# Kernel optimization log

Hardware: AMD Instinct MI355X
Metric: run time of the kernel (lower is better)

The kernel has to match this reference:

```python
import jax, jax.numpy as jnp
import numpy as np


def setup_inputs() -> dict:
    key = jax.random.key(0)
    k1, k2, k3, k4 = jax.random.split(key, 4)
    N, D, H = 16384, 128, 256
    features = jax.random.normal(k1, (N, D), dtype=jnp.float32)
    adj_matrix = jax.random.randint(k2, (N, N), 0, 2, dtype=jnp.int32)
    # Linear(2D -> H) and Linear(D -> H), torch convention W: [out, in]
    Wd = jax.random.normal(k3, (H, 2 * D), dtype=jnp.float32) * (1.0 / np.sqrt(2 * D))
    bd = jnp.zeros((H,), dtype=jnp.float32)
    Wo = jax.random.normal(k4, (H, D), dtype=jnp.float32) * (1.0 / np.sqrt(D))
    bo = jnp.zeros((H,), dtype=jnp.float32)
    return {"features": features, "adj_matrix": adj_matrix,
            "Wd": Wd, "bd": bd, "Wo": Wo, "bo": bo}


def reference(features, adj_matrix, Wd, bd, Wo, bo):
    # Faithful math, but without materializing the O(N^2*2D) pairwise tensor:
    #   sum_j adj[i,j] * concat(f[i], f[j]) = concat(deg[i]*f[i], (adj @ f)[i])
    adj = adj_matrix.astype(features.dtype)
    deg = jnp.sum(adj, axis=-1, keepdims=True)              # [N,1]
    neigh_mask = jnp.max(adj, axis=-1, keepdims=True)       # [N,1]
    neigh_num = deg + (1.0 - neigh_mask)                    # avoid div by 0
    head_sum = features * deg                                # [N,D]
    tail_sum = adj @ features                                # [N,D]
    neigh_ave = jnp.concatenate([head_sum, tail_sum], axis=-1) / neigh_num  # [N,2D]
    neigh_feat = neigh_ave @ Wd.T + bd                       # [N,H]
    updated = (features @ Wo.T + bo) - neigh_feat            # [N,H]
    updated = jnp.tanh(updated)
    # dropout is identity in eval mode; withAgg=False returns the pair
    return (updated, updated)
```

## Files before the change

### kernel.cpp

```cpp
#include <hip/hip_runtime.h>
#include <hip/hip_bf16.h>

#define NROW 16384
#define DIM 128
#define HOUT 256
#define SPLIT 4

typedef float f32x4 __attribute__((ext_vector_type(4)));
typedef __bf16 bf16x8 __attribute__((ext_vector_type(8)));
typedef int v4i __attribute__((ext_vector_type(4)));
typedef unsigned int u32;
typedef unsigned int u32x4 __attribute__((ext_vector_type(4)));

__global__ void k_transpose(const float* __restrict__ f, short* __restrict__ fT,
                            float* __restrict__ deg) {
    __shared__ short tr[128][72];
    const int t = threadIdx.x;
    const int j0 = blockIdx.x * 64;
    if (blockIdx.x < 64) deg[blockIdx.x * 256 + t] = 0.f;
    for (int it = 0; it < 8; ++it) {
        int slot = t + 256 * it;
        int j = slot >> 5;
        int dq = slot & 31;
        f32x4 v = *reinterpret_cast<const f32x4*>(f + (size_t)(j0 + j) * DIM + dq * 4);
#pragma unroll
        for (int c = 0; c < 4; ++c) {
            __hip_bfloat16 h = __float2bfloat16(v[c]);
            tr[dq * 4 + c][j] = *reinterpret_cast<short*>(&h);
        }
    }
    __syncthreads();
    for (int it = 0; it < 4; ++it) {
        int slot = t + 256 * it;
        int d = slot >> 3;
        int c8 = slot & 7;
        int4 v = *reinterpret_cast<const int4*>(&tr[d][c8 * 8]);
        *reinterpret_cast<int4*>(fT + (size_t)d * NROW + j0 + c8 * 8) = v;
    }
}

__device__ inline bf16x8 cvt8(v4i a, v4i b, int& ds) {
    union { u32x4 u; bf16x8 f; } U;
    U.u[0] = (a[0] ? 0x3F80u : 0u) | (a[1] ? 0x3F800000u : 0u);
    U.u[1] = (a[2] ? 0x3F80u : 0u) | (a[3] ? 0x3F800000u : 0u);
    U.u[2] = (b[0] ? 0x3F80u : 0u) | (b[1] ? 0x3F800000u : 0u);
    U.u[3] = (b[2] ? 0x3F80u : 0u) | (b[3] ? 0x3F800000u : 0u);
    ds += a[0] + a[1] + a[2] + a[3] + b[0] + b[1] + b[2] + b[3];
    return U.f;
}

#define GLOAD16(g, l)                                                         \
    __builtin_amdgcn_global_load_lds(                                         \
        (const __attribute__((address_space(1))) unsigned int*)(g),           \
        (__attribute__((address_space(3))) unsigned int*)(l), 16, 0, 0)

__global__ __launch_bounds__(256, 2) void k_gemm(const int* __restrict__ adj,
                                                 const short* __restrict__ fT,
                                                 float* __restrict__ part,
                                                 float* __restrict__ deg) {
    __shared__ int   As[2][128][32];
    __shared__ short Fs[2][128][32];
    const int t = threadIdx.x;
    const int rb = blockIdx.x >> 2;
    const int s  = blockIdx.x & 3;
    const int i0 = rb * 128;
    const int kb0 = s * (NROW / SPLIT);
    const int lane = t & 63;
    const int w = t >> 6;
    const int lr = lane & 15;
    const int lk8 = lane >> 4;

    f32x4 acc[2][8] = {};
    int dsum0 = 0, dsum1 = 0;

#define STAGE(cur, kb)                                                            \
    do {                                                                          \
        _Pragma("unroll")                                                         \
        for (int r = 0; r < 4; ++r) {                                             \
            int uslot = r * 256 + w * 64;                                         \
            int slot = uslot + lane;                                              \
            const int* g = adj + (size_t)(i0 + (slot >> 3)) * NROW + (kb) + (slot & 7) * 4; \
            GLOAD16(g, (char*)&As[cur][0][0] + (size_t)uslot * 16);               \
        }                                                                         \
        _Pragma("unroll")                                                         \
        for (int r = 0; r < 2; ++r) {                                             \
            int uslot = r * 256 + w * 64;                                         \
            int slot = uslot + lane;                                              \
            const short* g = fT + (size_t)(slot >> 2) * NROW + (kb) + (slot & 3) * 8; \
            GLOAD16(g, (char*)&Fs[cur][0][0] + (size_t)uslot * 16);               \
        }                                                                         \
    } while (0)

    STAGE(0, kb0);
    __syncthreads();

    int cur = 0;
#pragma unroll 1
    for (int step = 0; step < 128; ++step) {
        if (step + 1 < 128) STAGE(cur ^ 1, kb0 + (step + 1) * 32);
        bf16x8 bfr[8];
#pragma unroll
        for (int ci = 0; ci < 8; ++ci)
            bfr[ci] = *reinterpret_cast<const bf16x8*>(&Fs[cur][ci * 16 + lr][lk8 * 8]);
        v4i a0 = *reinterpret_cast<const v4i*>(&As[cur][w * 32 + lr][lk8 * 8]);
        v4i a1 = *reinterpret_cast<const v4i*>(&As[cur][w * 32 + lr][lk8 * 8 + 4]);
        v4i a2 = *reinterpret_cast<const v4i*>(&As[cur][w * 32 + 16 + lr][lk8 * 8]);
        v4i a3 = *reinterpret_cast<const v4i*>(&As[cur][w * 32 + 16 + lr][lk8 * 8 + 4]);
        bf16x8 af0 = cvt8(a0, a1, dsum0);
        bf16x8 af1 = cvt8(a2, a3, dsum1);
#pragma unroll
        for (int ci = 0; ci < 8; ++ci) {
            acc[0][ci] = __builtin_amdgcn_mfma_f32_16x16x32_bf16(af0, bfr[ci], acc[0][ci], 0, 0, 0);
            acc[1][ci] = __builtin_amdgcn_mfma_f32_16x16x32_bf16(af1, bfr[ci], acc[1][ci], 0, 0, 0);
        }
        __syncthreads();
        cur ^= 1;
    }

#pragma unroll
    for (int ti = 0; ti < 2; ++ti)
#pragma unroll
        for (int ci = 0; ci < 8; ++ci)
#pragma unroll
            for (int r = 0; r < 4; ++r) {
                int i = i0 + w * 32 + ti * 16 + (lane >> 4) * 4 + r;
                int d = ci * 16 + lr;
                part[((size_t)s * NROW + i) * DIM + d] = acc[ti][ci][r];
            }
    {
        float v0 = (float)dsum0;
        v0 += __shfl_xor(v0, 16);
        v0 += __shfl_xor(v0, 32);
        float v1 = (float)dsum1;
        v1 += __shfl_xor(v1, 16);
        v1 += __shfl_xor(v1, 32);
        if (lane < 16) {
            atomicAdd(deg + i0 + w * 32 + lr, v0);
            atomicAdd(deg + i0 + w * 32 + 16 + lr, v1);
        }
    }
#undef STAGE
}

__global__ __launch_bounds__(256, 2) void k_epilogue(const float* __restrict__ feat,
                                                     const float* __restrict__ part,
                                                     const float* __restrict__ deg,
                                                     const float* __restrict__ Wd,
                                                     const float* __restrict__ bd,
                                                     const float* __restrict__ Wo,
                                                     const float* __restrict__ bo,
                                                     float* __restrict__ out) {
    __shared__ float fs[32][132];
    __shared__ float tn[32][132];
    __shared__ float mrow[32], inv[32];
    const int t = threadIdx.x;
    const int i0 = blockIdx.x * 32;
    if (t < 32) {
        float d = deg[i0 + t];
        mrow[t] = d > 0.f ? 1.f : 0.f;
        inv[t]  = d > 0.f ? 1.f / d : 1.f;
    }
    __syncthreads();
    for (int it = 0; it < 4; ++it) {
        int slot = t + 256 * it;
        int r = slot >> 5, dq = slot & 31;
        size_t gi = (size_t)(i0 + r) * DIM + dq * 4;
        f32x4 fv = *reinterpret_cast<const f32x4*>(feat + gi);
        *reinterpret_cast<f32x4*>(&fs[r][dq * 4]) = fv;
        f32x4 p = *reinterpret_cast<const f32x4*>(part + gi);
#pragma unroll
        for (int sp = 1; sp < SPLIT; ++sp)
            p += *reinterpret_cast<const f32x4*>(part + (size_t)sp * NROW * DIM + gi);
        f32x4 tv = p * inv[r];
        *reinterpret_cast<f32x4*>(&tn[r][dq * 4]) = tv;
    }
    __syncthreads();
    const int rt = t & 7;
    const int ht = t >> 3;
    float accM[4][8] = {};
    float accB[4][8] = {};
    for (int d = 0; d < DIM; d += 4) {
        f32x4 fr[4], tr[4];
#pragma unroll
        for (int rr = 0; rr < 4; ++rr) {
            fr[rr] = *reinterpret_cast<const f32x4*>(&fs[rt * 4 + rr][d]);
            tr[rr] = *reinterpret_cast<const f32x4*>(&tn[rt * 4 + rr][d]);
        }
#pragma unroll
        for (int hh = 0; hh < 8; ++hh) {
            int h = ht * 8 + hh;
            f32x4 wo = *reinterpret_cast<const f32x4*>(Wo + (size_t)h * DIM + d);
            f32x4 w1 = *reinterpret_cast<const f32x4*>(Wd + (size_t)h * 2 * DIM + d);
            f32x4 w2 = *reinterpret_cast<const f32x4*>(Wd + (size_t)h * 2 * DIM + DIM + d);
#pragma unroll
            for (int rr = 0; rr < 4; ++rr)
#pragma unroll
                for (int c = 0; c < 4; ++c) {
                    accM[rr][hh] += fr[rr][c] * wo[c] - tr[rr][c] * w2[c];
                    accB[rr][hh] += fr[rr][c] * w1[c];
                }
        }
    }
    f32x4 bo0 = *reinterpret_cast<const f32x4*>(bo + ht * 8);
    f32x4 bo1 = *reinterpret_cast<const f32x4*>(bo + ht * 8 + 4);
    f32x4 bd0 = *reinterpret_cast<const f32x4*>(bd + ht * 8);
    f32x4 bd1 = *reinterpret_cast<const f32x4*>(bd + ht * 8 + 4);
#pragma unroll
    for (int rr = 0; rr < 4; ++rr) {
        int i = i0 + rt * 4 + rr;
        float m = mrow[rt * 4 + rr];
        f32x4 v0, v1;
#pragma unroll
        for (int c = 0; c < 4; ++c) {
            v0[c] = tanhf(accM[rr][c]     - m * accB[rr][c]     + bo0[c] - bd0[c]);
            v1[c] = tanhf(accM[rr][c + 4] - m * accB[rr][c + 4] + bo1[c] - bd1[c]);
        }
        float* o = out + (size_t)i * HOUT + ht * 8;
        *reinterpret_cast<f32x4*>(o) = v0;
        *reinterpret_cast<f32x4*>(o + 4) = v1;
        float* o2 = o + (size_t)NROW * HOUT;
        *reinterpret_cast<f32x4*>(o2) = v0;
        *reinterpret_cast<f32x4*>(o2 + 4) = v1;
    }
}

extern "C" void kernel_launch(void* const* d_in, const int* in_sizes, int n_in,
                              void* d_out, int out_size, void* d_ws, size_t ws_size,
                              hipStream_t stream) {
    const float* feat = (const float*)d_in[0];
    const int*   adj  = (const int*)d_in[1];
    const float* Wd   = (const float*)d_in[2];
    const float* bd   = (const float*)d_in[3];
    const float* Wo   = (const float*)d_in[4];
    const float* bo   = (const float*)d_in[5];
    float* out = (float*)d_out;
    char* ws = (char*)d_ws;
    short* fT   = (short*)ws;
    float* part = (float*)(ws + (size_t)4  * 1024 * 1024);
    float* deg  = (float*)(ws + (size_t)40 * 1024 * 1024);
    k_transpose<<<256, 256, 0, stream>>>(feat, fT, deg);
    k_gemm     <<<512, 256, 0, stream>>>(adj, fT, part, deg);
    k_epilogue <<<512, 256, 0, stream>>>(feat, part, deg, Wd, bd, Wo, bo, out);
}
```

Before: 1.431 ms.

## Retile adjacency GEMM to 64-row K64 tiles with XOR-swizzled LDS

Changes the GEMM block tile from 128 rows by 32 K to 64 rows by 64 K and doubles the grid. Adds XOR swizzling to the LDS layouts of both the adjacency and feature tiles to avoid bank conflicts on fragment reads. This gives longer contiguous global reads per row and more blocks, at the cost of re-reading the transposed features twice as often and using more LDS per block.

Result: slower. 1.490 ms (+4.1%).

```diff
diff --git a/kernel.cpp b/kernel.cpp
--- a/kernel.cpp
+++ b/kernel.cpp
@@ -58,37 +58,42 @@
                                                  const short* __restrict__ fT,
                                                  float* __restrict__ part,
                                                  float* __restrict__ deg) {
-    __shared__ int   As[2][128][32];
-    __shared__ short Fs[2][128][32];
+    __shared__ int   As[2][64][64];
+    __shared__ short Fs[2][128][64];
     const int t = threadIdx.x;
     const int rb = blockIdx.x >> 2;
     const int s  = blockIdx.x & 3;
-    const int i0 = rb * 128;
+    const int i0 = rb * 64;
     const int kb0 = s * (NROW / SPLIT);
     const int lane = t & 63;
     const int w = t >> 6;
     const int lr = lane & 15;
     const int lk8 = lane >> 4;
-
-    f32x4 acc[2][8] = {};
-    int dsum0 = 0, dsum1 = 0;
-
-#define STAGE(cur, kb)                                                            \
-    do {                                                                          \
-        _Pragma("unroll")                                                         \
-        for (int r = 0; r < 4; ++r) {                                             \
-            int uslot = r * 256 + w * 64;                                         \
-            int slot = uslot + lane;                                              \
-            const int* g = adj + (size_t)(i0 + (slot >> 3)) * NROW + (kb) + (slot & 7) * 4; \
-            GLOAD16(g, (char*)&As[cur][0][0] + (size_t)uslot * 16);               \
-        }                                                                         \
-        _Pragma("unroll")                                                         \
-        for (int r = 0; r < 2; ++r) {                                             \
-            int uslot = r * 256 + w * 64;                                         \
-            int slot = uslot + lane;                                              \
-            const short* g = fT + (size_t)(slot >> 2) * NROW + (kb) + (slot & 3) * 8; \
-            GLOAD16(g, (char*)&Fs[cur][0][0] + (size_t)uslot * 16);               \
-        }                                                                         \
+    const int sw = (lr & 7) << 4;
+
+    f32x4 acc[8] = {};
+    int dsum = 0;
+
+#define STAGE(cur, kb)                                                             \
+    do {                                                                           \
+        _Pragma("unroll")                                                          \
+        for (int r = 0; r < 4; ++r) {                                              \
+            int uslot = r * 256 + w * 64;                                          \
+            int slot = uslot + lane;                                               \
+            int row = slot >> 4;                                                   \
+            int c4 = (slot & 15) ^ (row & 7);                                      \
+            GLOAD16(adj + (size_t)(i0 + row) * NROW + (kb) + c4 * 4,               \
+                    (char*)&As[cur][0][0] + (size_t)uslot * 16);                   \
+        }                                                                          \
+        _Pragma("unroll")                                                          \
+        for (int r = 0; r < 4; ++r) {                                              \
+            int uslot = r * 256 + w * 64;                                          \
+            int slot = uslot + lane;                                               \
+            int d = slot >> 3;                                                     \
+            int c8 = (slot & 7) ^ (d & 7);                                         \
+            GLOAD16(fT + (size_t)d * NROW + (kb) + c8 * 8,                         \
+                    (char*)&Fs[cur][0][0] + (size_t)uslot * 16);                   \
+        }                                                                          \
     } while (0)
 
     STAGE(0, kb0);
@@ -96,48 +101,41 @@
 
     int cur = 0;
 #pragma unroll 1
-    for (int step = 0; step < 128; ++step) {
-        if (step + 1 < 128) STAGE(cur ^ 1, kb0 + (step + 1) * 32);
-        bf16x8 bfr[8];
-#pragma unroll
-        for (int ci = 0; ci < 8; ++ci)
-            bfr[ci] = *reinterpret_cast<const bf16x8*>(&Fs[cur][ci * 16 + lr][lk8 * 8]);
-        v4i a0 = *reinterpret_cast<const v4i*>(&As[cur][w * 32 + lr][lk8 * 8]);
-        v4i a1 = *reinterpret_cast<const v4i*>(&As[cur][w * 32 + lr][lk8 * 8 + 4]);
-        v4i a2 = *reinterpret_cast<const v4i*>(&As[cur][w * 32 + 16 + lr][lk8 * 8]);
-        v4i a3 = *reinterpret_cast<const v4i*>(&As[cur][w * 32 + 16 + lr][lk8 * 8 + 4]);
-        bf16x8 af0 = cvt8(a0, a1, dsum0);
-        bf16x8 af1 = cvt8(a2, a3, dsum1);
-#pragma unroll
-        for (int ci = 0; ci < 8; ++ci) {
-            acc[0][ci] = __builtin_amdgcn_mfma_f32_16x16x32_bf16(af0, bfr[ci], acc[0][ci], 0, 0, 0);
-            acc[1][ci] = __builtin_amdgcn_mfma_f32_16x16x32_bf16(af1, bfr[ci], acc[1][ci], 0, 0, 0);
+    for (int step = 0; step < 64; ++step) {
+        if (step + 1 < 64) STAGE(cur ^ 1, kb0 + (step + 1) * 64);
+        const char* Ab = (const char*)&As[cur][0][0] + (w * 16 + lr) * 256;
+        const char* Fb = (const char*)&Fs[cur][0][0];
+#pragma unroll
+        for (int kk = 0; kk < 2; ++kk) {
+            int xb = kk * 128 + lk8 * 32;
+            v4i a0 = *reinterpret_cast<const v4i*>(Ab + ((xb) ^ sw));
+            v4i a1 = *reinterpret_cast<const v4i*>(Ab + ((xb + 16) ^ sw));
+            bf16x8 af = cvt8(a0, a1, dsum);
+            int cb = kk * 64 + lk8 * 16;
+#pragma unroll
+            for (int ci = 0; ci < 8; ++ci) {
+                bf16x8 b = *reinterpret_cast<const bf16x8*>(
+                    Fb + (ci * 16 + lr) * 128 + (cb ^ sw));
+                acc[ci] = __builtin_amdgcn_mfma_f32_16x16x32_bf16(af, b, acc[ci], 0, 0, 0);
+            }
         }
         __syncthreads();
         cur ^= 1;
     }
 
 #pragma unroll
-    for (int ti = 0; ti < 2; ++ti)
-#pragma unroll
-        for (int ci = 0; ci < 8; ++ci)
-#pragma unroll
-            for (int r = 0; r < 4; ++r) {
-                int i = i0 + w * 32 + ti * 16 + (lane >> 4) * 4 + r;
-                int d = ci * 16 + lr;
-                part[((size_t)s * NROW + i) * DIM + d] = acc[ti][ci][r];
-            }
+    for (int ci = 0; ci < 8; ++ci)
+#pragma unroll
+        for (int r = 0; r < 4; ++r) {
+            int i = i0 + w * 16 + (lane >> 4) * 4 + r;
+            int d = ci * 16 + lr;
+            part[((size_t)s * NROW + i) * DIM + d] = acc[ci][r];
+        }
     {
-        float v0 = (float)dsum0;
-        v0 += __shfl_xor(v0, 16);
-        v0 += __shfl_xor(v0, 32);
-        float v1 = (float)dsum1;
-        v1 += __shfl_xor(v1, 16);
-        v1 += __shfl_xor(v1, 32);
-        if (lane < 16) {
-            atomicAdd(deg + i0 + w * 32 + lr, v0);
-            atomicAdd(deg + i0 + w * 32 + 16 + lr, v1);
-        }
+        float v = (float)dsum;
+        v += __shfl_xor(v, 16);
+        v += __shfl_xor(v, 32);
+        if (lane < 16) atomicAdd(deg + i0 + w * 16 + lr, v);
     }
 #undef STAGE
 }
@@ -238,7 +236,7 @@
     short* fT   = (short*)ws;
     float* part = (float*)(ws + (size_t)4  * 1024 * 1024);
     float* deg  = (float*)(ws + (size_t)40 * 1024 * 1024);
-    k_transpose<<<256, 256, 0, stream>>>(feat, fT, deg);
-    k_gemm     <<<512, 256, 0, stream>>>(adj, fT, part, deg);
-    k_epilogue <<<512, 256, 0, stream>>>(feat, part, deg, Wd, bd, Wo, bo, out);
-}
+    k_transpose<<<256,  256, 0, stream>>>(feat, fT, deg);
+    k_gemm     <<<1024, 256, 0, stream>>>(adj, fT, part, deg);
+    k_epilogue <<<512,  256, 0, stream>>>(feat, part, deg, Wd, bd, Wo, bo, out);
+}
```
